# Performance work log

Measured on AMD Instinct MI355X. Metric: run time of the kernel, lower is better.

## Reference

```python
import jax, jax.numpy as jnp
import numpy as np

B, T, I, H = 64, 512, 256, 512


def setup_inputs() -> dict:
    key = jax.random.key(0)
    ks = jax.random.split(key, 5)
    s = 1.0 / np.sqrt(H)  # PyTorch RNN init: U(-1/sqrt(H), 1/sqrt(H))
    x = jax.random.normal(ks[0], (B, T, I), dtype=jnp.float32)
    W_ih0 = jax.random.uniform(ks[1], (H, I), minval=-s, maxval=s, dtype=jnp.float32)
    W_hh0 = jax.random.uniform(ks[2], (H, H), minval=-s, maxval=s, dtype=jnp.float32)
    W_ih1 = jax.random.uniform(ks[3], (H, H), minval=-s, maxval=s, dtype=jnp.float32)
    W_hh1 = jax.random.uniform(ks[4], (H, H), minval=-s, maxval=s, dtype=jnp.float32)
    return {"x": x, "W_ih0": W_ih0, "W_hh0": W_hh0, "W_ih1": W_ih1, "W_hh1": W_hh1}


def _rnn_layer(inp, Wih, Whh):
    # Precompute input projection for all timesteps at once (one big GEMM).
    xw = jnp.einsum('bti,hi->bth', inp, Wih)  # [B, T, H]

    def step(h, xt):
        h = jnp.tanh(xt + h @ Whh.T)
        return h, h

    h0 = jnp.zeros((inp.shape[0], Whh.shape[0]), dtype=inp.dtype)
    _, ys = jax.lax.scan(step, h0, jnp.swapaxes(xw, 0, 1))  # scan over time
    return jnp.swapaxes(ys, 0, 1)  # [B, T, H]


def reference(x, W_ih0, W_hh0, W_ih1, W_hh1):
    # num_layers=2 stacked tanh RNN, bias=False, batch_first, zero initial state
    out = _rnn_layer(x, W_ih0, W_hh0)
    out = _rnn_layer(out, W_ih1, W_hh1)
    return out
```

## Files before the change

kernel.cpp:

```cpp
#include <hip/hip_runtime.h>
#include <math.h>

#define B   64
#define T   512
#define I0  256
#define H   512
#define M   (B*T)

#define NGR 4
#define BGR 16
#define NCH 16
#define CCH 32
#define HS_STRIDE 520

#define RSLOTS 8
#define RING_US ((size_t)RSLOTS * B * H)

typedef __attribute__((ext_vector_type(8))) short short8;
typedef __attribute__((ext_vector_type(4))) float floatx4;

static __device__ __forceinline__ unsigned short f2bf(float f) {
  unsigned u = __float_as_uint(f);
  u += 0x7fff + ((u >> 16) & 1);
  return (unsigned short)(u >> 16);
}
static __device__ __forceinline__ float bf2f(unsigned short u) {
  return __uint_as_float((unsigned)u << 16);
}
static __device__ __forceinline__ float ftanh(float x) {
  float e = __expf(2.0f * x);
  return 1.0f - 2.0f * __builtin_amdgcn_rcpf(e + 1.0f);
}

__global__ __launch_bounds__(256)
void pack_w(const float* __restrict__ W, unsigned short* __restrict__ dst) {
  int idx = blockIdx.x * 256 + threadIdx.x;
  int l = idx & 63, i = (idx >> 6) & 15, tau = (idx >> 10) & 1, c = idx >> 11;
  int col = c * CCH + tau * 16 + (l & 15);
  int k0  = i * 32 + (l >> 4) * 8;
  const float* src = &W[col * H + k0];
  unsigned v[4];
  #pragma unroll
  for (int j = 0; j < 4; ++j) {
    unsigned lo = f2bf(src[2*j]);
    unsigned hi = f2bf(src[2*j + 1]);
    v[j] = lo | (hi << 16);
  }
  *(uint4*)&dst[(size_t)idx * 8] = make_uint4(v[0], v[1], v[2], v[3]);
}

__global__ __launch_bounds__(256)
void pack_wx(const float* __restrict__ W, unsigned short* __restrict__ dst) {
  int idx = blockIdx.x * 256 + threadIdx.x;
  int l = idx & 63, kt = (idx >> 6) & 7, t = idx >> 9;
  int col = t * 16 + (l & 15);
  int k0  = kt * 32 + (l >> 4) * 8;
  const float* src = &W[col * I0 + k0];
  unsigned v[4];
  #pragma unroll
  for (int j = 0; j < 4; ++j) {
    unsigned lo = f2bf(src[2*j]);
    unsigned hi = f2bf(src[2*j + 1]);
    v[j] = lo | (hi << 16);
  }
  *(uint4*)&dst[(size_t)idx * 8] = make_uint4(v[0], v[1], v[2], v[3]);
}

__global__ __launch_bounds__(256)
void gemm_mfma(const float* __restrict__ x, const unsigned short* __restrict__ wpx,
               unsigned short* __restrict__ xwb) {
  extern __shared__ unsigned short wl[];
  const int tid = threadIdx.x, wv = tid >> 6, lane = tid & 63;
  const int mrow = lane & 15, quad = lane >> 4;
  const int m0 = blockIdx.x * 64 + wv * 16;
  const int n0 = blockIdx.y * 256;
  {
    const uint4* s = (const uint4*)(wpx + (size_t)(n0 / 16) * 4096);
    uint4* d = (uint4*)wl;
    for (int i = tid; i < 8192; i += 256) d[i] = s[i];
  }
  short8 ah[8], al[8];
  const float* xr = x + (size_t)(m0 + mrow) * I0;
  #pragma unroll
  for (int kt = 0; kt < 8; ++kt) {
    float4 u = *(const float4*)&xr[kt * 32 + quad * 8];
    float4 v = *(const float4*)&xr[kt * 32 + quad * 8 + 4];
    float f[8] = {u.x,u.y,u.z,u.w,v.x,v.y,v.z,v.w};
    union { unsigned w[4]; short8 s; } hi, lo;
    #pragma unroll
    for (int j = 0; j < 4; ++j) {
      unsigned short h0 = f2bf(f[2*j]),   l0 = f2bf(f[2*j]   - bf2f(h0));
      unsigned short h1 = f2bf(f[2*j+1]), l1 = f2bf(f[2*j+1] - bf2f(h1));
      hi.w[j] = (unsigned)h0 | ((unsigned)h1 << 16);
      lo.w[j] = (unsigned)l0 | ((unsigned)l1 << 16);
    }
    ah[kt] = hi.s; al[kt] = lo.s;
  }
  __syncthreads();
  for (int ct = 0; ct < 16; ++ct) {
    floatx4 acc = {0.f,0.f,0.f,0.f};
    #pragma unroll
    for (int kt = 0; kt < 8; ++kt) {
      short8 b = *(const short8*)(wl + ((size_t)(ct * 8 + kt) * 64 + lane) * 8);
      acc = __builtin_amdgcn_mfma_f32_16x16x32_bf16(al[kt], b, acc, 0, 0, 0);
      acc = __builtin_amdgcn_mfma_f32_16x16x32_bf16(ah[kt], b, acc, 0, 0, 0);
    }
    #pragma unroll
    for (int i = 0; i < 4; ++i)
      xwb[(size_t)(m0 + quad*4 + i) * H + n0 + ct*16 + mrow] = f2bf(acc[i]);
  }
}

__global__ __launch_bounds__(256)
void rnn_fused(const unsigned short* __restrict__ xwb,
               const unsigned short* __restrict__ wp0,
               const unsigned short* __restrict__ wp1,
               const unsigned short* __restrict__ wp2,
               unsigned short* __restrict__ ring0,
               unsigned short* __restrict__ ring1,
               float* __restrict__ dout)
{
  extern __shared__ unsigned short smem[];
  unsigned short* Ws0 = smem;
  unsigned short* Wi1 = Ws0 + 16384;
  unsigned short* Ws1 = Wi1 + 16384;
  unsigned short* hs0 = Ws1 + 16384;
  unsigned short* hs1 = hs0 + 8320;

  const int tid   = threadIdx.x;
  const int g     = blockIdx.x & 3;
  const int chunk = blockIdx.x >> 2;
  const int c0    = chunk * CCH;
  const int b0    = g * BGR;
  const int wv    = tid >> 6;
  const int lane  = tid & 63;
  const int mrow  = lane & 15;
  const int quad  = lane >> 4;

  {
    const uint4* s0 = (const uint4*)(wp0 + (size_t)chunk * 16384);
    const uint4* s1 = (const uint4*)(wp1 + (size_t)chunk * 16384);
    const uint4* s2 = (const uint4*)(wp2 + (size_t)chunk * 16384);
    uint4* d0 = (uint4*)Ws0; uint4* d1 = (uint4*)Wi1; uint4* d2 = (uint4*)Ws1;
    for (int i = tid; i < 2048; i += 256) { d0[i] = s0[i]; d1[i] = s1[i]; d2[i] = s2[i]; }
  }
  for (int i = tid; i < 2080; i += 256) ((unsigned long long*)hs1)[i] = 0ULL;
  __syncthreads();

  long cnt = 0;

  for (int r = 0; r <= T; ++r) {
    unsigned short xus[4];
    if (wv < 2 && r < T) {
      const int ccol = c0 + wv * 16 + mrow;
      #pragma unroll
      for (int i = 0; i < 4; ++i)
        xus[i] = xwb[((size_t)(b0 + quad * 4 + i) * T + r) * H + ccol];
    }

    unsigned long long v0[8], v1[8];
    if (r >= 1) {
      const unsigned long long* s0 =
          (const unsigned long long*)(ring0 + (size_t)((r - 1) & (RSLOTS - 1)) * (B * H))
          + b0 * 128;
      const unsigned long long* s1 =
          (const unsigned long long*)(ring1 + (size_t)((r - 2) & (RSLOTS - 1)) * (B * H))
          + b0 * 128;
      const bool need1 = (r >= 2);
      for (;;) {
        #pragma unroll
        for (int j = 0; j < 8; ++j)
          v0[j] = __hip_atomic_load(s0 + j * 256 + tid,
                                    __ATOMIC_RELAXED, __HIP_MEMORY_SCOPE_AGENT);
        if (need1) {
          #pragma unroll
          for (int j = 0; j < 8; ++j)
            v1[j] = __hip_atomic_load(s1 + j * 256 + tid,
                                      __ATOMIC_RELAXED, __HIP_MEMORY_SCOPE_AGENT);
        }
        unsigned long long bad = 0;
        #pragma unroll
        for (int j = 0; j < 8; ++j) {
          unsigned long long w = ~v0[j];
          bad |= (w - 0x0001000100010001ULL) & ~w & 0x8000800080008000ULL;
        }
        if (need1) {
          #pragma unroll
          for (int j = 0; j < 8; ++j) {
            unsigned long long w = ~v1[j];
            bad |= (w - 0x0001000100010001ULL) & ~w & 0x8000800080008000ULL;
          }
        }
        if (bad == 0 || ++cnt > 2000000L) break;
      }
      #pragma unroll
      for (int j = 0; j < 8; ++j) {
        int ii = j * 256 + tid, row = ii >> 7, c8 = ii & 127;
        *(unsigned long long*)&hs0[row * HS_STRIDE + c8 * 4] = v0[j];
      }
      if (need1) {
        #pragma unroll
        for (int j = 0; j < 8; ++j) {
          int ii = j * 256 + tid, row = ii >> 7, c8 = ii & 127;
          *(unsigned long long*)&hs1[row * HS_STRIDE + c8 * 4] = v1[j];
        }
      }
    }
    asm volatile("s_waitcnt lgkmcnt(0)\n\ts_barrier" ::: "memory");
    __builtin_amdgcn_sched_barrier(0);

    if (wv < 2) {
      if (r < T) {
        floatx4 acc = {0.f, 0.f, 0.f, 0.f};
        if (r >= 1) {
          const unsigned short* wb = Ws0 + wv * 8192;
          const unsigned short* ha = hs0 + mrow * HS_STRIDE + quad * 8;
          #pragma unroll
          for (int i = 0; i < 16; ++i) {
            short8 a = *(const short8*)(ha + i * 32);
            short8 b = *(const short8*)(wb + (i * 64 + lane) * 8);
            acc = __builtin_amdgcn_mfma_f32_16x16x32_bf16(a, b, acc, 0, 0, 0);
          }
        }
        const int ccol = c0 + wv * 16 + mrow;
        unsigned short* rdst = ring0 + (size_t)(r & (RSLOTS - 1)) * (B * H);
        unsigned short* rrst = ring0 + (size_t)((r + 4) & (RSLOTS - 1)) * (B * H);
        #pragma unroll
        for (int i = 0; i < 4; ++i) {
          int b = b0 + quad * 4 + i;
          float h = ftanh(acc[i] + bf2f(xus[i]));
          __hip_atomic_store(rdst + (size_t)b * H + ccol, f2bf(h),
                             __ATOMIC_RELAXED, __HIP_MEMORY_SCOPE_AGENT);
        }
        #pragma unroll
        for (int i = 0; i < 4; ++i) {
          int b = b0 + quad * 4 + i;
          __hip_atomic_store(rrst + (size_t)b * H + ccol, (unsigned short)0xFFFFu,
                             __ATOMIC_RELAXED, __HIP_MEMORY_SCOPE_AGENT);
        }
      }
    } else {
      if (r >= 1) {
        floatx4 acc = {0.f, 0.f, 0.f, 0.f};
        const int tt = wv - 2;
        const unsigned short* wi  = Wi1 + tt * 8192;
        const unsigned short* wh  = Ws1 + tt * 8192;
        const unsigned short* ha0 = hs0 + mrow * HS_STRIDE + quad * 8;
        const unsigned short* ha1 = hs1 + mrow * HS_STRIDE + quad * 8;
        #pragma unroll
        for (int i = 0; i < 16; ++i) {
          short8 a = *(const short8*)(ha0 + i * 32);
          short8 b = *(const short8*)(wi + (i * 64 + lane) * 8);
          acc = __builtin_amdgcn_mfma_f32_16x16x32_bf16(a, b, acc, 0, 0, 0);
        }
        #pragma unroll
        for (int i = 0; i < 16; ++i) {
          short8 a = *(const short8*)(ha1 + i * 32);
          short8 b = *(const short8*)(wh + (i * 64 + lane) * 8);
          acc = __builtin_amdgcn_mfma_f32_16x16x32_bf16(a, b, acc, 0, 0, 0);
        }
        const int ccol = c0 + tt * 16 + mrow;
        const int t2 = r - 1;
        unsigned short* rdst = ring1 + (size_t)(t2 & (RSLOTS - 1)) * (B * H);
        unsigned short* rrst = ring1 + (size_t)((t2 + 4) & (RSLOTS - 1)) * (B * H);
        float hv[4];
        #pragma unroll
        for (int i = 0; i < 4; ++i) {
          int b = b0 + quad * 4 + i;
          float h = ftanh(acc[i]);
          hv[i] = h;
          __hip_atomic_store(rdst + (size_t)b * H + ccol, f2bf(h),
                             __ATOMIC_RELAXED, __HIP_MEMORY_SCOPE_AGENT);
        }
        #pragma unroll
        for (int i = 0; i < 4; ++i) {
          int b = b0 + quad * 4 + i;
          dout[((size_t)b * T + t2) * H + ccol] = hv[i];
          __hip_atomic_store(rrst + (size_t)b * H + ccol, (unsigned short)0xFFFFu,
                             __ATOMIC_RELAXED, __HIP_MEMORY_SCOPE_AGENT);
        }
      }
    }
    asm volatile("s_barrier" ::: "memory");
  }
}

#define SMEM_BYTES ((3 * 16384 + 2 * 8320) * 2)
#define SMEM_GEMM  131072

extern "C" void kernel_launch(void* const* d_in, const int* in_sizes, int n_in,
                              void* d_out, int out_size, void* d_ws, size_t ws_size,
                              hipStream_t stream) {
  const float* x    = (const float*)d_in[0];
  const float* Wih0 = (const float*)d_in[1];
  const float* Whh0 = (const float*)d_in[2];
  const float* Wih1 = (const float*)d_in[3];
  const float* Whh1 = (const float*)d_in[4];
  float* out = (float*)d_out;

  char* ws = (char*)d_ws;
  unsigned short* xwb = (unsigned short*)ws;
  unsigned short* wp0 = (unsigned short*)(ws + (size_t)32*1024*1024);
  unsigned short* wp1 = (unsigned short*)(ws + (size_t)32*1024*1024 + 512*1024);
  unsigned short* wp2 = (unsigned short*)(ws + (size_t)32*1024*1024 + 1024*1024);
  unsigned short* wpx = (unsigned short*)(ws + (size_t)32*1024*1024 + 1536*1024);
  unsigned short* ring0 = (unsigned short*)(ws + (size_t)32*1024*1024 + 1792*1024);
  unsigned short* ring1 = ring0 + RING_US;

  hipMemsetAsync(ring0, 0xFF, 2 * RING_US * sizeof(unsigned short), stream);
  hipFuncSetAttribute((const void*)rnn_fused,
                      hipFuncAttributeMaxDynamicSharedMemorySize, SMEM_BYTES);
  hipFuncSetAttribute((const void*)gemm_mfma,
                      hipFuncAttributeMaxDynamicSharedMemorySize, SMEM_GEMM);

  pack_w<<<128, 256, 0, stream>>>(Whh0, wp0);
  pack_w<<<128, 256, 0, stream>>>(Wih1, wp1);
  pack_w<<<128, 256, 0, stream>>>(Whh1, wp2);
  pack_wx<<<64, 256, 0, stream>>>(Wih0, wpx);

  dim3 gg(M/64, H/256);
  gemm_mfma<<<gg, 256, SMEM_GEMM, stream>>>(x, wpx, xwb);

  rnn_fused<<<NGR * NCH, 256, SMEM_BYTES, stream>>>(
      xwb, wp0, wp1, wp2, ring0, ring1, out);
}
```

Before: 1.217 ms.

## Hold recurrent weights in registers, double-buffer swizzled hidden state, fuse pack kernels

New measurement: 1.200 ms. No clear change (-1.5%).

```diff
diff --git a/kernel.cpp b/kernel.cpp
--- a/kernel.cpp
+++ b/kernel.cpp
@@ -11,13 +11,13 @@
 #define BGR 16
 #define NCH 16
 #define CCH 32
-#define HS_STRIDE 520
 
 #define RSLOTS 8
 #define RING_US ((size_t)RSLOTS * B * H)
 
 typedef __attribute__((ext_vector_type(8))) short short8;
 typedef __attribute__((ext_vector_type(4))) float floatx4;
+typedef unsigned long long u64;
 
 static __device__ __forceinline__ unsigned short f2bf(float f) {
   unsigned u = __float_as_uint(f);
@@ -33,52 +33,51 @@
 }
 
 __global__ __launch_bounds__(256)
-void pack_w(const float* __restrict__ W, unsigned short* __restrict__ dst) {
-  int idx = blockIdx.x * 256 + threadIdx.x;
-  int l = idx & 63, i = (idx >> 6) & 15, tau = (idx >> 10) & 1, c = idx >> 11;
-  int col = c * CCH + tau * 16 + (l & 15);
-  int k0  = i * 32 + (l >> 4) * 8;
-  const float* src = &W[col * H + k0];
-  unsigned v[4];
-  #pragma unroll
-  for (int j = 0; j < 4; ++j) {
-    unsigned lo = f2bf(src[2*j]);
-    unsigned hi = f2bf(src[2*j + 1]);
-    v[j] = lo | (hi << 16);
-  }
-  *(uint4*)&dst[(size_t)idx * 8] = make_uint4(v[0], v[1], v[2], v[3]);
-}
-
-__global__ __launch_bounds__(256)
-void pack_wx(const float* __restrict__ W, unsigned short* __restrict__ dst) {
-  int idx = blockIdx.x * 256 + threadIdx.x;
-  int l = idx & 63, kt = (idx >> 6) & 7, t = idx >> 9;
-  int col = t * 16 + (l & 15);
-  int k0  = kt * 32 + (l >> 4) * 8;
-  const float* src = &W[col * I0 + k0];
-  unsigned v[4];
-  #pragma unroll
-  for (int j = 0; j < 4; ++j) {
-    unsigned lo = f2bf(src[2*j]);
-    unsigned hi = f2bf(src[2*j + 1]);
-    v[j] = lo | (hi << 16);
-  }
-  *(uint4*)&dst[(size_t)idx * 8] = make_uint4(v[0], v[1], v[2], v[3]);
+void pack_all(const float* __restrict__ Whh0, const float* __restrict__ Wih1,
+              const float* __restrict__ Whh1, const float* __restrict__ Wih0,
+              unsigned short* __restrict__ wp0, unsigned short* __restrict__ wp1,
+              unsigned short* __restrict__ wp2, unsigned short* __restrict__ wpx) {
+  const int bk = blockIdx.x, tid = threadIdx.x;
+  if (bk < 384) {
+    const float* W = (bk < 128) ? Whh0 : (bk < 256) ? Wih1 : Whh1;
+    unsigned short* dst = (bk < 128) ? wp0 : (bk < 256) ? wp1 : wp2;
+    int idx = (bk & 127) * 256 + tid;
+    int l = idx & 63, i = (idx >> 6) & 15, tau = (idx >> 10) & 1, c = idx >> 11;
+    int col = c * CCH + tau * 16 + (l & 15);
+    int k0  = i * 32 + (l >> 4) * 8;
+    const float* src = &W[col * H + k0];
+    unsigned v[4];
+    #pragma unroll
+    for (int j = 0; j < 4; ++j) {
+      unsigned lo = f2bf(src[2*j]);
+      unsigned hi = f2bf(src[2*j + 1]);
+      v[j] = lo | (hi << 16);
+    }
+    *(uint4*)&dst[(size_t)idx * 8] = make_uint4(v[0], v[1], v[2], v[3]);
+  } else {
+    int idx = (bk - 384) * 256 + tid;
+    int l = idx & 63, kt = (idx >> 6) & 7, t = idx >> 9;
+    int col = t * 16 + (l & 15);
+    int k0  = kt * 32 + (l >> 4) * 8;
+    const float* src = &Wih0[col * I0 + k0];
+    unsigned v[4];
+    #pragma unroll
+    for (int j = 0; j < 4; ++j) {
+      unsigned lo = f2bf(src[2*j]);
+      unsigned hi = f2bf(src[2*j + 1]);
+      v[j] = lo | (hi << 16);
+    }
+    *(uint4*)&wpx[(size_t)idx * 8] = make_uint4(v[0], v[1], v[2], v[3]);
+  }
 }
 
 __global__ __launch_bounds__(256)
 void gemm_mfma(const float* __restrict__ x, const unsigned short* __restrict__ wpx,
                unsigned short* __restrict__ xwb) {
-  extern __shared__ unsigned short wl[];
   const int tid = threadIdx.x, wv = tid >> 6, lane = tid & 63;
   const int mrow = lane & 15, quad = lane >> 4;
   const int m0 = blockIdx.x * 64 + wv * 16;
   const int n0 = blockIdx.y * 256;
-  {
-    const uint4* s = (const uint4*)(wpx + (size_t)(n0 / 16) * 4096);
-    uint4* d = (uint4*)wl;
-    for (int i = tid; i < 8192; i += 256) d[i] = s[i];
-  }
   short8 ah[8], al[8];
   const float* xr = x + (size_t)(m0 + mrow) * I0;
   #pragma unroll
@@ -96,12 +95,12 @@
     }
     ah[kt] = hi.s; al[kt] = lo.s;
   }
-  __syncthreads();
   for (int ct = 0; ct < 16; ++ct) {
+    const unsigned short* wb = wpx + (size_t)(n0 / 16 + ct) * 4096;
     floatx4 acc = {0.f,0.f,0.f,0.f};
     #pragma unroll
     for (int kt = 0; kt < 8; ++kt) {
-      short8 b = *(const short8*)(wl + ((size_t)(ct * 8 + kt) * 64 + lane) * 8);
+      short8 b = *(const short8*)(wb + ((size_t)(kt * 64 + lane)) * 8);
       acc = __builtin_amdgcn_mfma_f32_16x16x32_bf16(al[kt], b, acc, 0, 0, 0);
       acc = __builtin_amdgcn_mfma_f32_16x16x32_bf16(ah[kt], b, acc, 0, 0, 0);
     }
@@ -121,11 +120,9 @@
                float* __restrict__ dout)
 {
   extern __shared__ unsigned short smem[];
-  unsigned short* Ws0 = smem;
-  unsigned short* Wi1 = Ws0 + 16384;
-  unsigned short* Ws1 = Wi1 + 16384;
-  unsigned short* hs0 = Ws1 + 16384;
-  unsigned short* hs1 = hs0 + 8320;
+  unsigned short* Wi1 = smem;
+  unsigned short* hs0 = Wi1 + 16384;
+  unsigned short* hs1 = hs0 + 16384;
 
   const int tid   = threadIdx.x;
   const int g     = blockIdx.x & 3;
@@ -138,13 +135,19 @@
   const int quad  = lane >> 4;
 
   {
-    const uint4* s0 = (const uint4*)(wp0 + (size_t)chunk * 16384);
     const uint4* s1 = (const uint4*)(wp1 + (size_t)chunk * 16384);
-    const uint4* s2 = (const uint4*)(wp2 + (size_t)chunk * 16384);
-    uint4* d0 = (uint4*)Ws0; uint4* d1 = (uint4*)Wi1; uint4* d2 = (uint4*)Ws1;
-    for (int i = tid; i < 2048; i += 256) { d0[i] = s0[i]; d1[i] = s1[i]; d2[i] = s2[i]; }
-  }
-  for (int i = tid; i < 2080; i += 256) ((unsigned long long*)hs1)[i] = 0ULL;
+    uint4* d1 = (uint4*)Wi1;
+    for (int i = tid; i < 2048; i += 256) d1[i] = s1[i];
+  }
+  short8 wreg[16];
+  {
+    const unsigned short* wsrc = (wv < 2) ? wp0 : wp2;
+    const int tvg = chunk * 2 + (wv & 1);
+    #pragma unroll
+    for (int kt = 0; kt < 16; ++kt)
+      wreg[kt] = *(const short8*)(wsrc + (size_t)((tvg*16 + kt)*64 + lane) * 8);
+  }
+  for (int i = tid; i < 4096; i += 256) ((u64*)hs1)[i] = 0ULL;
   __syncthreads();
 
   long cnt = 0;
@@ -158,15 +161,15 @@
         xus[i] = xwb[((size_t)(b0 + quad * 4 + i) * T + r) * H + ccol];
     }
 
-    unsigned long long v0[8], v1[8];
+    u64 v0[8], v1[8];
+    const bool need1 = (r >= 2);
     if (r >= 1) {
-      const unsigned long long* s0 =
-          (const unsigned long long*)(ring0 + (size_t)((r - 1) & (RSLOTS - 1)) * (B * H))
+      const u64* s0 =
+          (const u64*)(ring0 + (size_t)((r - 1) & (RSLOTS - 1)) * (B * H))
           + b0 * 128;
-      const unsigned long long* s1 =
-          (const unsigned long long*)(ring1 + (size_t)((r - 2) & (RSLOTS - 1)) * (B * H))
+      const u64* s1 =
+          (const u64*)(ring1 + (size_t)((r - 2) & (RSLOTS - 1)) * (B * H))
           + b0 * 128;
-      const bool need1 = (r >= 2);
       for (;;) {
         #pragma unroll
         for (int j = 0; j < 8; ++j)
@@ -178,31 +181,38 @@
             v1[j] = __hip_atomic_load(s1 + j * 256 + tid,
                                       __ATOMIC_RELAXED, __HIP_MEMORY_SCOPE_AGENT);
         }
-        unsigned long long bad = 0;
+        u64 bad = 0;
         #pragma unroll
         for (int j = 0; j < 8; ++j) {
-          unsigned long long w = ~v0[j];
+          u64 w = ~v0[j];
           bad |= (w - 0x0001000100010001ULL) & ~w & 0x8000800080008000ULL;
         }
         if (need1) {
           #pragma unroll
           for (int j = 0; j < 8; ++j) {
-            unsigned long long w = ~v1[j];
+            u64 w = ~v1[j];
             bad |= (w - 0x0001000100010001ULL) & ~w & 0x8000800080008000ULL;
           }
         }
         if (bad == 0 || ++cnt > 2000000L) break;
       }
+      const int p = r & 1;
+      u64* H0 = (u64*)hs0 + p * 2048;
       #pragma unroll
       for (int j = 0; j < 8; ++j) {
         int ii = j * 256 + tid, row = ii >> 7, c8 = ii & 127;
-        *(unsigned long long*)&hs0[row * HS_STRIDE + c8 * 4] = v0[j];
+        int kt = c8 >> 3, q2 = (c8 & 7) >> 1;
+        int slot = kt * 64 + q2 * 16 + row;
+        H0[(((slot ^ (kt & 7)) << 1) | (c8 & 1))] = v0[j];
       }
       if (need1) {
+        u64* H1 = (u64*)hs1 + p * 2048;
         #pragma unroll
         for (int j = 0; j < 8; ++j) {
           int ii = j * 256 + tid, row = ii >> 7, c8 = ii & 127;
-          *(unsigned long long*)&hs1[row * HS_STRIDE + c8 * 4] = v1[j];
+          int kt = c8 >> 3, q2 = (c8 & 7) >> 1;
+          int slot = kt * 64 + q2 * 16 + row;
+          H1[(((slot ^ (kt & 7)) << 1) | (c8 & 1))] = v1[j];
         }
       }
     }
@@ -213,13 +223,11 @@
       if (r < T) {
         floatx4 acc = {0.f, 0.f, 0.f, 0.f};
         if (r >= 1) {
-          const unsigned short* wb = Ws0 + wv * 8192;
-          const unsigned short* ha = hs0 + mrow * HS_STRIDE + quad * 8;
+          const unsigned short* hb = hs0 + (r & 1) * 8192;
           #pragma unroll
-          for (int i = 0; i < 16; ++i) {
-            short8 a = *(const short8*)(ha + i * 32);
-            short8 b = *(const short8*)(wb + (i * 64 + lane) * 8);
-            acc = __builtin_amdgcn_mfma_f32_16x16x32_bf16(a, b, acc, 0, 0, 0);
+          for (int kt = 0; kt < 16; ++kt) {
+            short8 a = *(const short8*)(hb + ((size_t)((kt*64 + lane) ^ (kt & 7))) * 8);
+            acc = __builtin_amdgcn_mfma_f32_16x16x32_bf16(a, wreg[kt], acc, 0, 0, 0);
           }
         }
         const int ccol = c0 + wv * 16 + mrow;
@@ -244,20 +252,18 @@
         floatx4 acc = {0.f, 0.f, 0.f, 0.f};
         const int tt = wv - 2;
         const unsigned short* wi  = Wi1 + tt * 8192;
-        const unsigned short* wh  = Ws1 + tt * 8192;
-        const unsigned short* ha0 = hs0 + mrow * HS_STRIDE + quad * 8;
-        const unsigned short* ha1 = hs1 + mrow * HS_STRIDE + quad * 8;
-        #pragma unroll
-        for (int i = 0; i < 16; ++i) {
-          short8 a = *(const short8*)(ha0 + i * 32);
-          short8 b = *(const short8*)(wi + (i * 64 + lane) * 8);
+        const unsigned short* hb0 = hs0 + (r & 1) * 8192;
+        const unsigned short* hb1 = hs1 + (r & 1) * 8192;
+        #pragma unroll
+        for (int kt = 0; kt < 16; ++kt) {
+          short8 a = *(const short8*)(hb0 + ((size_t)((kt*64 + lane) ^ (kt & 7))) * 8);
+          short8 b = *(const short8*)(wi + ((size_t)(kt * 64 + lane)) * 8);
           acc = __builtin_amdgcn_mfma_f32_16x16x32_bf16(a, b, acc, 0, 0, 0);
         }
         #pragma unroll
-        for (int i = 0; i < 16; ++i) {
-          short8 a = *(const short8*)(ha1 + i * 32);
-          short8 b = *(const short8*)(wh + (i * 64 + lane) * 8);
-          acc = __builtin_amdgcn_mfma_f32_16x16x32_bf16(a, b, acc, 0, 0, 0);
+        for (int kt = 0; kt < 16; ++kt) {
+          short8 a = *(const short8*)(hb1 + ((size_t)((kt*64 + lane) ^ (kt & 7))) * 8);
+          acc = __builtin_amdgcn_mfma_f32_16x16x32_bf16(a, wreg[kt], acc, 0, 0, 0);
         }
         const int ccol = c0 + tt * 16 + mrow;
         const int t2 = r - 1;
@@ -281,12 +287,10 @@
         }
       }
     }
-    asm volatile("s_barrier" ::: "memory");
-  }
-}
-
-#define SMEM_BYTES ((3 * 16384 + 2 * 8320) * 2)
-#define SMEM_GEMM  131072
+  }
+}
+
+#define SMEM_BYTES ((16384 + 16384 + 16384) * 2)
 
 extern "C" void kernel_launch(void* const* d_in, const int* in_sizes, int n_in,
                               void* d_out, int out_size, void* d_ws, size_t ws_size,
@@ -310,16 +314,11 @@
   hipMemsetAsync(ring0, 0xFF, 2 * RING_US * sizeof(unsigned short), stream);
   hipFuncSetAttribute((const void*)rnn_fused,
                       hipFuncAttributeMaxDynamicSharedMemorySize, SMEM_BYTES);
-  hipFuncSetAttribute((const void*)gemm_mfma,
-                      hipFuncAttributeMaxDynamicSharedMemorySize, SMEM_GEMM);
-
-  pack_w<<<128, 256, 0, stream>>>(Whh0, wp0);
-  pack_w<<<128, 256, 0, stream>>>(Wih1, wp1);
-  pack_w<<<128, 256, 0, stream>>>(Whh1, wp2);
-  pack_wx<<<64, 256, 0, stream>>>(Wih0, wpx);
+
+  pack_all<<<448, 256, 0, stream>>>(Whh0, Wih1, Whh1, Wih0, wp0, wp1, wp2, wpx);
 
   dim3 gg(M/64, H/256);
-  gemm_mfma<<<gg, 256, SMEM_GEMM, stream>>>(x, wpx, xwb);
+  gemm_mfma<<<gg, 256, 0, stream>>>(x, wpx, xwb);
 
   rnn_fused<<<NGR * NCH, 256, SMEM_BYTES, stream>>>(
       xwb, wp0, wp1, wp2, ring0, ring1, out);
```
